# Optimization experiments

Hardware: AMD Instinct MI355X
Metric: run time of the kernel (lower is better)

Reference implementation:

```python
import jax, jax.numpy as jnp
import numpy as np

H_IMG, W_IMG = 32, 32   # image_size -> seq_len = 1024
NH, HD, D = 8, 32, 256  # num_heads, head_dim, d_model
B = 8


def _relative_positions(h, w):
    # Swin-style relative position index table, [h*w, h*w] int32
    y = np.arange(h); x = np.arange(w)
    coords = np.stack(np.meshgrid(y, x, indexing='ij')).reshape(2, -1)  # [2, S]
    rel = coords[:, :, None] - coords[:, None, :]                      # [2, S, S]
    rel = rel.transpose(1, 2, 0).astype(np.int64)                      # [S, S, 2]
    rel[:, :, 0] += h - 1
    rel[:, :, 1] += w - 1
    rel[:, :, 0] *= 2 * w - 1
    return np.int32(rel.sum(-1))                                       # [S, S]

_POS = _relative_positions(H_IMG, W_IMG)


def setup_inputs() -> dict:
    key = jax.random.key(0)
    ks = jax.random.split(key, 8)
    S = H_IMG * W_IMG
    return {
        'inputs_q': jax.random.normal(ks[0], (B, S, D), jnp.float32),
        'inputs_kv': jax.random.normal(ks[1], (B, S, D), jnp.float32),
        'Wq': jax.random.normal(ks[2], (D, NH, HD), jnp.float32) / np.sqrt(D),
        'bq': jnp.zeros((NH, HD), jnp.float32),
        'Wk': jax.random.normal(ks[3], (D, NH, HD), jnp.float32) / np.sqrt(D),
        'bk': jnp.zeros((NH, HD), jnp.float32),
        'Wv': jax.random.normal(ks[4], (D, NH, HD), jnp.float32) / np.sqrt(D),
        'bv': jnp.zeros((NH, HD), jnp.float32),
        'rel_table': 0.02 * jax.random.normal(ks[5], ((2 * H_IMG - 1) * (2 * W_IMG - 1), NH), jnp.float32),
        'Wo': jax.random.normal(ks[6], (NH, HD, D), jnp.float32) / np.sqrt(NH * HD),
        'bo': jnp.zeros((D,), jnp.float32),
    }


def reference(inputs_q, inputs_kv, Wq, bq, Wk, bk, Wv, bv, rel_table, Wo, bo):
    pos = jnp.asarray(_POS)                                  # [S, S] int32 (constant)
    q = jnp.einsum('bsd,dhk->bshk', inputs_q, Wq) + bq       # [B, S, H, HD]
    k = jnp.einsum('bsd,dhk->bshk', inputs_kv, Wk) + bk
    v = jnp.einsum('bsd,dhk->bshk', inputs_kv, Wv) + bv
    q = q / jnp.sqrt(jnp.asarray(HD, q.dtype))
    attn = jnp.einsum('bqhd,bkhd->bhqk', q, k)               # [B, H, S, S]
    rel_bias = rel_table[pos]                                # [S, S, H]
    attn = attn + jnp.transpose(rel_bias, (2, 0, 1))[None]   # broadcast over batch
    attn = jax.nn.softmax(attn, axis=-1)
    x = jnp.einsum('bhqk,bkhd->bqhd', attn, v)               # [B, S, H, HD]
    return jnp.einsum('bqhd,hdf->bqf', x, Wo) + bo           # [B, S, D]
```

## Files before the change

### kernel.cpp

```cpp
#include <hip/hip_runtime.h>
#include <hip/hip_bf16.h>

#define B_SZ   8
#define S_LEN  1024
#define D_MOD  256
#define NHEADS 8
#define HDIM   32
#define H_IMG  32
#define W_IMG  32
#define M_ROWS (B_SZ * S_LEN)

typedef _Float16 f16x8 __attribute__((ext_vector_type(8)));
typedef _Float16 f16x4 __attribute__((ext_vector_type(4)));
typedef float    f32x4 __attribute__((ext_vector_type(4)));

__device__ inline f16x8 load8_f16(const float* p) {
    f32x4 a = *(const f32x4*)p;
    f32x4 b = *(const f32x4*)(p + 4);
    f16x8 r;
    r[0] = (_Float16)a[0]; r[1] = (_Float16)a[1];
    r[2] = (_Float16)a[2]; r[3] = (_Float16)a[3];
    r[4] = (_Float16)b[0]; r[5] = (_Float16)b[1];
    r[6] = (_Float16)b[2]; r[7] = (_Float16)b[3];
    return r;
}
__device__ inline f16x8 load8_f16(const _Float16* p) { return *(const f16x8*)p; }

__global__ __launch_bounds__(256)
void wtrans_kernel(const float* __restrict__ Wq, const float* __restrict__ Wk,
                   const float* __restrict__ Wv, const float* __restrict__ Wo,
                   _Float16* __restrict__ wt) {
    const int mi = blockIdx.x >> 3;
    const int k0 = (blockIdx.x & 7) << 5;
    const float* W = (mi == 0) ? Wq : (mi == 1) ? Wk : (mi == 2) ? Wv : Wo;
    const int n = threadIdx.x;
    const float* src = W + (size_t)k0 * 256 + n;
    _Float16* dst = wt + (size_t)mi * 65536 + (size_t)n * 256 + k0;
#pragma unroll
    for (int g = 0; g < 4; ++g) {
        f16x8 o;
#pragma unroll
        for (int j = 0; j < 8; ++j) o[j] = (_Float16)src[(size_t)(g * 8 + j) * 256];
        *(f16x8*)(dst + g * 8) = o;
    }
}

template <typename InT, typename OutT>
__device__ inline void gemm_body(const InT* __restrict__ A, const _Float16* __restrict__ Wt,
                                 const float* __restrict__ bias, OutT* __restrict__ out,
                                 float scale, int m0, int n0) {
    __shared__ _Float16 As[64][136];
    __shared__ _Float16 Bt[64][136];
    const int tid  = threadIdx.x;
    const int w    = tid >> 6;
    const int lane = tid & 63;
    const int quad = lane >> 4;
    const int l16  = lane & 15;
    const int mq   = (w & 1) * 32;
    const int nq   = (w >> 1) * 32;

    f32x4 acc[2][2];
#pragma unroll
    for (int i = 0; i < 2; ++i)
#pragma unroll
        for (int j = 0; j < 2; ++j) acc[i][j] = (f32x4){0.f, 0.f, 0.f, 0.f};

#pragma unroll
    for (int ks = 0; ks < 2; ++ks) {
        if (ks) __syncthreads();
#pragma unroll
        for (int i = 0; i < 4; ++i) {
            const int idx = i * 2048 + tid * 8;
            const int r = idx >> 7, c = idx & 127;
            *(f16x8*)(&As[r][c]) = load8_f16(A + (size_t)(m0 + r) * 256 + ks * 128 + c);
            *(f16x8*)(&Bt[r][c]) = *(const f16x8*)(Wt + (size_t)(n0 + r) * 256 + ks * 128 + c);
        }
        __syncthreads();
#pragma unroll
        for (int kk = 0; kk < 4; ++kk) {
            const int k8 = kk * 32 + quad * 8;
            f16x8 a0 = *(const f16x8*)(&As[mq + l16][k8]);
            f16x8 a1 = *(const f16x8*)(&As[mq + 16 + l16][k8]);
            f16x8 b0 = *(const f16x8*)(&Bt[nq + l16][k8]);
            f16x8 b1 = *(const f16x8*)(&Bt[nq + 16 + l16][k8]);
            acc[0][0] = __builtin_amdgcn_mfma_f32_16x16x32_f16(a0, b0, acc[0][0], 0, 0, 0);
            acc[0][1] = __builtin_amdgcn_mfma_f32_16x16x32_f16(a0, b1, acc[0][1], 0, 0, 0);
            acc[1][0] = __builtin_amdgcn_mfma_f32_16x16x32_f16(a1, b0, acc[1][0], 0, 0, 0);
            acc[1][1] = __builtin_amdgcn_mfma_f32_16x16x32_f16(a1, b1, acc[1][1], 0, 0, 0);
        }
    }

#pragma unroll
    for (int nh = 0; nh < 2; ++nh) {
        const int col = n0 + nq + nh * 16 + l16;
        const float bv = bias[col];
#pragma unroll
        for (int mh = 0; mh < 2; ++mh) {
#pragma unroll
            for (int r = 0; r < 4; ++r) {
                const int row = m0 + mq + mh * 16 + quad * 4 + r;
                out[(size_t)row * 256 + col] = (OutT)((acc[mh][nh][r] + bv) * scale);
            }
        }
    }
}

__global__ __launch_bounds__(256)
void gemm_qkv_kernel(const float* __restrict__ in_q, const float* __restrict__ in_kv,
                     const _Float16* __restrict__ wt,
                     const float* __restrict__ bq, const float* __restrict__ bk,
                     const float* __restrict__ bv, _Float16* __restrict__ outbase,
                     float qscale) {
    const int z = blockIdx.z;
    const float* A    = (z == 0) ? in_q : in_kv;
    const float* bias = (z == 0) ? bq : (z == 1) ? bk : bv;
    _Float16* out = outbase + (size_t)z * M_ROWS * 256;
    const float scale = (z == 0) ? qscale : 1.0f;
    gemm_body<float, _Float16>(A, wt + (size_t)z * 65536, bias, out, scale,
                               blockIdx.x * 64, blockIdx.y * 64);
}

__global__ __launch_bounds__(256)
void gemm_out_kernel(const _Float16* __restrict__ X, const _Float16* __restrict__ wt,
                     const float* __restrict__ bo, float* __restrict__ out) {
    gemm_body<_Float16, float>(X, wt + (size_t)3 * 65536, bo, out, 1.0f,
                               blockIdx.x * 64, blockIdx.y * 64);
}

__global__ __launch_bounds__(256)
void attn_kernel(const _Float16* __restrict__ q, const _Float16* __restrict__ k,
                 const _Float16* __restrict__ v, const float* __restrict__ rel_table,
                 _Float16* __restrict__ xout) {
    __shared__ _Float16 Vt[2][32][40];
    __shared__ _Float16 Ps[4][16][40];
    __shared__ float    bias_row[4][64];

    const int tid  = threadIdx.x;
    const int w    = tid >> 6;
    const int lane = tid & 63;
    const int quad = lane >> 4;
    const int l16  = lane & 15;
    const int b    = blockIdx.z;
    const int h    = blockIdx.y;
    const int qrow_base = blockIdx.x * 64 + w * 16;
    const int yq      = qrow_base >> 5;
    const int xq_base = qrow_base & 31;

    const f16x8 q_frag =
        *(const f16x8*)(q + ((size_t)(b * S_LEN + qrow_base + l16)) * D_MOD + h * HDIM + quad * 8);

    const _Float16* kp0 = k + ((size_t)(b * S_LEN + l16)) * D_MOD + h * HDIM + quad * 8;

    const int vkey = tid >> 3;
    const int vhd  = (tid & 7) * 4;
    const _Float16* vp = v + ((size_t)(b * S_LEN + vkey)) * D_MOD + h * HDIM + vhd;

    const float* biasp = rel_table + ((size_t)(yq + 31) * 63 + lane) * NHEADS + h;

    f32x4 o_acc0 = (f32x4){0.f, 0.f, 0.f, 0.f};
    f32x4 o_acc1 = (f32x4){0.f, 0.f, 0.f, 0.f};
    float l_part[4] = {0.f, 0.f, 0.f, 0.f};

    {
        f16x4 v4 = *(const f16x4*)vp;
        Vt[0][vhd + 0][vkey] = v4[0];
        Vt[0][vhd + 1][vkey] = v4[1];
        Vt[0][vhd + 2][vkey] = v4[2];
        Vt[0][vhd + 3][vkey] = v4[3];
    }
    if (lane < 63) bias_row[w][lane] = biasp[0];
    __syncthreads();

    for (int kt = 0; kt < S_LEN / 32; ++kt) {
        const int cur = kt & 1;
        const bool more = (kt < S_LEN / 32 - 1);

        f16x4 vnext = (f16x4){0, 0, 0, 0};
        if (more) vnext = *(const f16x4*)(vp + (size_t)(kt + 1) * 32 * D_MOD);
        float bnext = 0.f;
        if (more && lane < 63) bnext = biasp[-(ptrdiff_t)(kt + 1) * 63 * NHEADS];

        const _Float16* kp = kp0 + (size_t)kt * 32 * D_MOD;
        const f16x8 kf0 = *(const f16x8*)kp;
        const f16x8 kf1 = *(const f16x8*)(kp + (size_t)16 * D_MOD);

        const f32x4 zero = (f32x4){0.f, 0.f, 0.f, 0.f};
        f32x4 s0 = __builtin_amdgcn_mfma_f32_16x16x32_f16(q_frag, kf0, zero, 0, 0, 0);
        f32x4 s1 = __builtin_amdgcn_mfma_f32_16x16x32_f16(q_frag, kf1, zero, 0, 0, 0);

#pragma unroll
        for (int r = 0; r < 4; ++r) {
            const int xq = xq_base + quad * 4 + r;
            const float p0 = __expf(s0[r] + bias_row[w][xq - l16 + 31]);
            const float p1 = __expf(s1[r] + bias_row[w][xq - l16 + 15]);
            l_part[r] += p0 + p1;
            const int ql = quad * 4 + r;
            Ps[w][ql][l16]      = (_Float16)p0;
            Ps[w][ql][l16 + 16] = (_Float16)p1;
        }

        const f16x8 pf  = *(const f16x8*)(&Ps[w][l16][quad * 8]);
        const f16x8 vf0 = *(const f16x8*)(&Vt[cur][l16][quad * 8]);
        const f16x8 vf1 = *(const f16x8*)(&Vt[cur][l16 + 16][quad * 8]);
        o_acc0 = __builtin_amdgcn_mfma_f32_16x16x32_f16(pf, vf0, o_acc0, 0, 0, 0);
        o_acc1 = __builtin_amdgcn_mfma_f32_16x16x32_f16(pf, vf1, o_acc1, 0, 0, 0);

        if (more) {
            const int nxt = cur ^ 1;
            Vt[nxt][vhd + 0][vkey] = vnext[0];
            Vt[nxt][vhd + 1][vkey] = vnext[1];
            Vt[nxt][vhd + 2][vkey] = vnext[2];
            Vt[nxt][vhd + 3][vkey] = vnext[3];
            if (lane < 63) bias_row[w][lane] = bnext;
        }
        __syncthreads();
    }

#pragma unroll
    for (int r = 0; r < 4; ++r) {
        float l = l_part[r];
        l += __shfl_xor(l, 1);
        l += __shfl_xor(l, 2);
        l += __shfl_xor(l, 4);
        l += __shfl_xor(l, 8);
        const float inv = 1.0f / l;
        const int qg = qrow_base + quad * 4 + r;
        const size_t base = ((size_t)(b * S_LEN + qg)) * D_MOD + h * HDIM;
        xout[base + l16]      = (_Float16)(o_acc0[r] * inv);
        xout[base + l16 + 16] = (_Float16)(o_acc1[r] * inv);
    }
}

extern "C" void kernel_launch(void* const* d_in, const int* in_sizes, int n_in,
                              void* d_out, int out_size, void* d_ws, size_t ws_size,
                              hipStream_t stream) {
    const float* in_q  = (const float*)d_in[0];
    const float* in_kv = (const float*)d_in[1];
    const float* Wq    = (const float*)d_in[2];
    const float* bq    = (const float*)d_in[3];
    const float* Wk    = (const float*)d_in[4];
    const float* bk    = (const float*)d_in[5];
    const float* Wv    = (const float*)d_in[6];
    const float* bv    = (const float*)d_in[7];
    const float* rel   = (const float*)d_in[8];
    const float* Wo    = (const float*)d_in[9];
    const float* bo    = (const float*)d_in[10];
    float* out = (float*)d_out;

    _Float16* qh = (_Float16*)d_ws;
    _Float16* kh = qh + (size_t)M_ROWS * D_MOD;
    _Float16* vh = kh + (size_t)M_ROWS * D_MOD;
    _Float16* xh = vh + (size_t)M_ROWS * D_MOD;
    _Float16* wt = xh + (size_t)M_ROWS * D_MOD;

    const dim3 blk(256);
    const float qscale = 0.17677669529663687f;

    wtrans_kernel<<<dim3(32), blk, 0, stream>>>(Wq, Wk, Wv, Wo, wt);
    gemm_qkv_kernel<<<dim3(M_ROWS / 64, 4, 3), blk, 0, stream>>>(
        in_q, in_kv, wt, bq, bk, bv, qh, qscale);
    attn_kernel<<<dim3(S_LEN / 64, NHEADS, B_SZ), blk, 0, stream>>>(qh, kh, vh, rel, xh);
    gemm_out_kernel<<<dim3(M_ROWS / 64, 4), blk, 0, stream>>>(xh, wt, bo, out);
}
```

Baseline: 147.9 us.

## Transpose V in QKV GEMM, restructure attention with exp2 and MFMA row sums

The QKV GEMM now double-buffers 64-wide K slices in shared memory and writes V transposed per (batch, head), so attention can load V fragments straight from global memory without an LDS transpose or block-wide barriers. Attention processes 32 query rows per wave, folds the bias into the MFMA accumulator input, uses exp2 with log2e pre-folded into the q scale and bias, and computes row sums with an extra MFMA against a ones vector. The grid is remapped so blocks of the same batch and head land on the same XCD. Risks include higher register pressure, fewer blocks in the attention launch, and per-wave Ps/bias buffers that rely on wave-level ordering without barriers.

```diff
diff --git a/kernel.cpp b/kernel.cpp
--- a/kernel.cpp
+++ b/kernel.cpp
@@ -5,26 +5,15 @@
 #define S_LEN  1024
 #define D_MOD  256
 #define NHEADS 8
-#define HDIM   32
 #define H_IMG  32
 #define W_IMG  32
 #define M_ROWS (B_SZ * S_LEN)
+#define LOG2E  1.4426950408889634f
+#define QSCALE_LOG2E 0.2550352766751165f
 
 typedef _Float16 f16x8 __attribute__((ext_vector_type(8)));
 typedef _Float16 f16x4 __attribute__((ext_vector_type(4)));
 typedef float    f32x4 __attribute__((ext_vector_type(4)));
-
-__device__ inline f16x8 load8_f16(const float* p) {
-    f32x4 a = *(const f32x4*)p;
-    f32x4 b = *(const f32x4*)(p + 4);
-    f16x8 r;
-    r[0] = (_Float16)a[0]; r[1] = (_Float16)a[1];
-    r[2] = (_Float16)a[2]; r[3] = (_Float16)a[3];
-    r[4] = (_Float16)b[0]; r[5] = (_Float16)b[1];
-    r[6] = (_Float16)b[2]; r[7] = (_Float16)b[3];
-    return r;
-}
-__device__ inline f16x8 load8_f16(const _Float16* p) { return *(const f16x8*)p; }
 
 __global__ __launch_bounds__(256)
 void wtrans_kernel(const float* __restrict__ Wq, const float* __restrict__ Wk,
@@ -45,12 +34,25 @@
     }
 }
 
-template <typename InT, typename OutT>
+__device__ inline void ldA16(const float* p, f16x8& x0, f16x8& x1) {
+    f32x4 a = *(const f32x4*)p, b = *(const f32x4*)(p + 4);
+    f32x4 c = *(const f32x4*)(p + 8), d = *(const f32x4*)(p + 12);
+#pragma unroll
+    for (int j = 0; j < 4; ++j) {
+        x0[j] = (_Float16)a[j]; x0[4 + j] = (_Float16)b[j];
+        x1[j] = (_Float16)c[j]; x1[4 + j] = (_Float16)d[j];
+    }
+}
+__device__ inline void ldA16(const _Float16* p, f16x8& x0, f16x8& x1) {
+    x0 = *(const f16x8*)p; x1 = *(const f16x8*)(p + 8);
+}
+
+template <typename InT, typename OutT, int VT_MODE>
 __device__ inline void gemm_body(const InT* __restrict__ A, const _Float16* __restrict__ Wt,
                                  const float* __restrict__ bias, OutT* __restrict__ out,
                                  float scale, int m0, int n0) {
-    __shared__ _Float16 As[64][136];
-    __shared__ _Float16 Bt[64][136];
+    __shared__ __align__(16) _Float16 As[2][64][72];
+    __shared__ __align__(16) _Float16 Bt[2][64][72];
     const int tid  = threadIdx.x;
     const int w    = tid >> 6;
     const int lane = tid & 63;
@@ -59,6 +61,20 @@
     const int mq   = (w & 1) * 32;
     const int nq   = (w >> 1) * 32;
 
+    const int srow = tid >> 2;
+    const int scol = (tid & 3) << 4;
+    const InT* Ap = A + (size_t)(m0 + srow) * 256 + scol;
+    const _Float16* Bp = Wt + (size_t)(n0 + srow) * 256 + scol;
+
+    f16x8 a0n, a1n, b0n, b1n;
+    ldA16(Ap, a0n, a1n);
+    b0n = *(const f16x8*)Bp; b1n = *(const f16x8*)(Bp + 8);
+    *(f16x8*)(&As[0][srow][scol])     = a0n;
+    *(f16x8*)(&As[0][srow][scol + 8]) = a1n;
+    *(f16x8*)(&Bt[0][srow][scol])     = b0n;
+    *(f16x8*)(&Bt[0][srow][scol + 8]) = b1n;
+    __syncthreads();
+
     f32x4 acc[2][2];
 #pragma unroll
     for (int i = 0; i < 2; ++i)
@@ -66,40 +82,63 @@
         for (int j = 0; j < 2; ++j) acc[i][j] = (f32x4){0.f, 0.f, 0.f, 0.f};
 
 #pragma unroll
-    for (int ks = 0; ks < 2; ++ks) {
-        if (ks) __syncthreads();
-#pragma unroll
-        for (int i = 0; i < 4; ++i) {
-            const int idx = i * 2048 + tid * 8;
-            const int r = idx >> 7, c = idx & 127;
-            *(f16x8*)(&As[r][c]) = load8_f16(A + (size_t)(m0 + r) * 256 + ks * 128 + c);
-            *(f16x8*)(&Bt[r][c]) = *(const f16x8*)(Wt + (size_t)(n0 + r) * 256 + ks * 128 + c);
-        }
-        __syncthreads();
-#pragma unroll
-        for (int kk = 0; kk < 4; ++kk) {
+    for (int s = 0; s < 4; ++s) {
+        const int cur = s & 1;
+        if (s < 3) {
+            ldA16(Ap + (s + 1) * 64, a0n, a1n);
+            b0n = *(const f16x8*)(Bp + (s + 1) * 64);
+            b1n = *(const f16x8*)(Bp + (s + 1) * 64 + 8);
+        }
+#pragma unroll
+        for (int kk = 0; kk < 2; ++kk) {
             const int k8 = kk * 32 + quad * 8;
-            f16x8 a0 = *(const f16x8*)(&As[mq + l16][k8]);
-            f16x8 a1 = *(const f16x8*)(&As[mq + 16 + l16][k8]);
-            f16x8 b0 = *(const f16x8*)(&Bt[nq + l16][k8]);
-            f16x8 b1 = *(const f16x8*)(&Bt[nq + 16 + l16][k8]);
-            acc[0][0] = __builtin_amdgcn_mfma_f32_16x16x32_f16(a0, b0, acc[0][0], 0, 0, 0);
-            acc[0][1] = __builtin_amdgcn_mfma_f32_16x16x32_f16(a0, b1, acc[0][1], 0, 0, 0);
-            acc[1][0] = __builtin_amdgcn_mfma_f32_16x16x32_f16(a1, b0, acc[1][0], 0, 0, 0);
-            acc[1][1] = __builtin_amdgcn_mfma_f32_16x16x32_f16(a1, b1, acc[1][1], 0, 0, 0);
-        }
-    }
-
-#pragma unroll
-    for (int nh = 0; nh < 2; ++nh) {
-        const int col = n0 + nq + nh * 16 + l16;
-        const float bv = bias[col];
-#pragma unroll
-        for (int mh = 0; mh < 2; ++mh) {
-#pragma unroll
-            for (int r = 0; r < 4; ++r) {
-                const int row = m0 + mq + mh * 16 + quad * 4 + r;
-                out[(size_t)row * 256 + col] = (OutT)((acc[mh][nh][r] + bv) * scale);
+            f16x8 fa0 = *(const f16x8*)(&As[cur][mq + l16][k8]);
+            f16x8 fa1 = *(const f16x8*)(&As[cur][mq + 16 + l16][k8]);
+            f16x8 fb0 = *(const f16x8*)(&Bt[cur][nq + l16][k8]);
+            f16x8 fb1 = *(const f16x8*)(&Bt[cur][nq + 16 + l16][k8]);
+            acc[0][0] = __builtin_amdgcn_mfma_f32_16x16x32_f16(fa0, fb0, acc[0][0], 0, 0, 0);
+            acc[0][1] = __builtin_amdgcn_mfma_f32_16x16x32_f16(fa0, fb1, acc[0][1], 0, 0, 0);
+            acc[1][0] = __builtin_amdgcn_mfma_f32_16x16x32_f16(fa1, fb0, acc[1][0], 0, 0, 0);
+            acc[1][1] = __builtin_amdgcn_mfma_f32_16x16x32_f16(fa1, fb1, acc[1][1], 0, 0, 0);
+        }
+        if (s < 3) {
+            const int nxt = cur ^ 1;
+            *(f16x8*)(&As[nxt][srow][scol])     = a0n;
+            *(f16x8*)(&As[nxt][srow][scol + 8]) = a1n;
+            *(f16x8*)(&Bt[nxt][srow][scol])     = b0n;
+            *(f16x8*)(&Bt[nxt][srow][scol + 8]) = b1n;
+            __syncthreads();
+        }
+    }
+
+    if (VT_MODE) {
+        const int b8 = (m0 >> 10) * 8;
+#pragma unroll
+        for (int nh = 0; nh < 2; ++nh) {
+            const int col = n0 + nq + nh * 16 + l16;
+            const float bv = bias[col];
+#pragma unroll
+            for (int mh = 0; mh < 2; ++mh) {
+                const int row0 = (m0 & 1023) + mq + mh * 16 + quad * 4;
+                f16x4 pk;
+#pragma unroll
+                for (int r = 0; r < 4; ++r) pk[r] = (_Float16)((acc[mh][nh][r] + bv) * scale);
+                *(f16x4*)((_Float16*)out +
+                          ((size_t)(b8 + (col >> 5)) * 32 + (col & 31)) * 1024 + row0) = pk;
+            }
+        }
+    } else {
+#pragma unroll
+        for (int nh = 0; nh < 2; ++nh) {
+            const int col = n0 + nq + nh * 16 + l16;
+            const float bv = bias[col];
+#pragma unroll
+            for (int mh = 0; mh < 2; ++mh) {
+#pragma unroll
+                for (int r = 0; r < 4; ++r) {
+                    const int row = m0 + mq + mh * 16 + quad * 4 + r;
+                    out[(size_t)row * 256 + col] = (OutT)((acc[mh][nh][r] + bv) * scale);
+                }
             }
         }
     }
@@ -109,125 +148,128 @@
 void gemm_qkv_kernel(const float* __restrict__ in_q, const float* __restrict__ in_kv,
                      const _Float16* __restrict__ wt,
                      const float* __restrict__ bq, const float* __restrict__ bk,
-                     const float* __restrict__ bv, _Float16* __restrict__ outbase,
-                     float qscale) {
+                     const float* __restrict__ bv,
+                     _Float16* __restrict__ qh, _Float16* __restrict__ kh,
+                     _Float16* __restrict__ vt) {
     const int z = blockIdx.z;
-    const float* A    = (z == 0) ? in_q : in_kv;
-    const float* bias = (z == 0) ? bq : (z == 1) ? bk : bv;
-    _Float16* out = outbase + (size_t)z * M_ROWS * 256;
-    const float scale = (z == 0) ? qscale : 1.0f;
-    gemm_body<float, _Float16>(A, wt + (size_t)z * 65536, bias, out, scale,
-                               blockIdx.x * 64, blockIdx.y * 64);
+    const int m0 = blockIdx.x * 64, n0 = blockIdx.y * 64;
+    if (z == 0)
+        gemm_body<float, _Float16, 0>(in_q, wt, bq, qh, QSCALE_LOG2E, m0, n0);
+    else if (z == 1)
+        gemm_body<float, _Float16, 0>(in_kv, wt + 65536, bk, kh, 1.0f, m0, n0);
+    else
+        gemm_body<float, _Float16, 1>(in_kv, wt + 2 * 65536, bv, vt, 1.0f, m0, n0);
 }
 
 __global__ __launch_bounds__(256)
 void gemm_out_kernel(const _Float16* __restrict__ X, const _Float16* __restrict__ wt,
                      const float* __restrict__ bo, float* __restrict__ out) {
-    gemm_body<_Float16, float>(X, wt + (size_t)3 * 65536, bo, out, 1.0f,
-                               blockIdx.x * 64, blockIdx.y * 64);
+    gemm_body<_Float16, float, 0>(X, wt + (size_t)3 * 65536, bo, out, 1.0f,
+                                  blockIdx.x * 64, blockIdx.y * 64);
 }
 
 __global__ __launch_bounds__(256)
 void attn_kernel(const _Float16* __restrict__ q, const _Float16* __restrict__ k,
-                 const _Float16* __restrict__ v, const float* __restrict__ rel_table,
+                 const _Float16* __restrict__ vt, const float* __restrict__ rel_table,
                  _Float16* __restrict__ xout) {
-    __shared__ _Float16 Vt[2][32][40];
-    __shared__ _Float16 Ps[4][16][40];
-    __shared__ float    bias_row[4][64];
+    __shared__ __align__(16) _Float16 Ps[4][2][32][40];
+    __shared__ float bias_row[4][2][64];
 
     const int tid  = threadIdx.x;
     const int w    = tid >> 6;
     const int lane = tid & 63;
     const int quad = lane >> 4;
     const int l16  = lane & 15;
-    const int b    = blockIdx.z;
-    const int h    = blockIdx.y;
-    const int qrow_base = blockIdx.x * 64 + w * 16;
-    const int yq      = qrow_base >> 5;
-    const int xq_base = qrow_base & 31;
-
-    const f16x8 q_frag =
-        *(const f16x8*)(q + ((size_t)(b * S_LEN + qrow_base + l16)) * D_MOD + h * HDIM + quad * 8);
-
-    const _Float16* kp0 = k + ((size_t)(b * S_LEN + l16)) * D_MOD + h * HDIM + quad * 8;
-
-    const int vkey = tid >> 3;
-    const int vhd  = (tid & 7) * 4;
-    const _Float16* vp = v + ((size_t)(b * S_LEN + vkey)) * D_MOD + h * HDIM + vhd;
-
-    const float* biasp = rel_table + ((size_t)(yq + 31) * 63 + lane) * NHEADS + h;
-
-    f32x4 o_acc0 = (f32x4){0.f, 0.f, 0.f, 0.f};
-    f32x4 o_acc1 = (f32x4){0.f, 0.f, 0.f, 0.f};
-    float l_part[4] = {0.f, 0.f, 0.f, 0.f};
-
-    {
-        f16x4 v4 = *(const f16x4*)vp;
-        Vt[0][vhd + 0][vkey] = v4[0];
-        Vt[0][vhd + 1][vkey] = v4[1];
-        Vt[0][vhd + 2][vkey] = v4[2];
-        Vt[0][vhd + 3][vkey] = v4[3];
-    }
-    if (lane < 63) bias_row[w][lane] = biasp[0];
-    __syncthreads();
+
+    const int n     = blockIdx.x;
+    const int xcd   = n & 7;
+    const int local = n >> 3;
+    const int bh    = xcd * 8 + (local & 7);
+    const int qc    = local >> 3;
+    const int b     = bh >> 3, h = bh & 7;
+    const int qrow_base = qc * 128 + w * 32;
+    const int yq = qrow_base >> 5;
+
+    const _Float16* qp = q + ((size_t)(b * S_LEN + qrow_base + l16)) * D_MOD + h * 32 + quad * 8;
+    const f16x8 qf0 = *(const f16x8*)(qp);
+    const f16x8 qf1 = *(const f16x8*)(qp + 16 * D_MOD);
+    const _Float16* kp = k + ((size_t)(b * S_LEN + l16)) * D_MOD + h * 32 + quad * 8;
+    const _Float16* vp = vt + ((size_t)(bh * 32 + l16)) * S_LEN + quad * 8;
+    const float* bp = rel_table + ((size_t)(yq + 31) * 63 + lane) * NHEADS + h;
+
+    f16x8 ones;
+#pragma unroll
+    for (int j = 0; j < 8; ++j) ones[j] = (_Float16)1.0f;
+
+    f32x4 o00 = {0.f,0.f,0.f,0.f}, o01 = {0.f,0.f,0.f,0.f};
+    f32x4 o10 = {0.f,0.f,0.f,0.f}, o11 = {0.f,0.f,0.f,0.f};
+    f32x4 ol0 = {0.f,0.f,0.f,0.f}, ol1 = {0.f,0.f,0.f,0.f};
+
+    if (lane < 63) bias_row[w][0][lane] = bp[0] * LOG2E;
+    f16x8 kf0 = *(const f16x8*)(kp);
+    f16x8 kf1 = *(const f16x8*)(kp + 16 * D_MOD);
+    f16x8 vf0 = *(const f16x8*)(vp);
+    f16x8 vf1 = *(const f16x8*)(vp + 16 * S_LEN);
 
     for (int kt = 0; kt < S_LEN / 32; ++kt) {
-        const int cur = kt & 1;
+        const int cur = kt & 1, nxt = cur ^ 1;
+        f16x8 nk0, nk1, nv0, nv1;
+        float nb = 0.f;
         const bool more = (kt < S_LEN / 32 - 1);
-
-        f16x4 vnext = (f16x4){0, 0, 0, 0};
-        if (more) vnext = *(const f16x4*)(vp + (size_t)(kt + 1) * 32 * D_MOD);
-        float bnext = 0.f;
-        if (more && lane < 63) bnext = biasp[-(ptrdiff_t)(kt + 1) * 63 * NHEADS];
-
-        const _Float16* kp = kp0 + (size_t)kt * 32 * D_MOD;
-        const f16x8 kf0 = *(const f16x8*)kp;
-        const f16x8 kf1 = *(const f16x8*)(kp + (size_t)16 * D_MOD);
-
-        const f32x4 zero = (f32x4){0.f, 0.f, 0.f, 0.f};
-        f32x4 s0 = __builtin_amdgcn_mfma_f32_16x16x32_f16(q_frag, kf0, zero, 0, 0, 0);
-        f32x4 s1 = __builtin_amdgcn_mfma_f32_16x16x32_f16(q_frag, kf1, zero, 0, 0, 0);
-
+        if (more) {
+            const _Float16* kq = kp + (size_t)(kt + 1) * 32 * D_MOD;
+            nk0 = *(const f16x8*)(kq);
+            nk1 = *(const f16x8*)(kq + 16 * D_MOD);
+            const _Float16* vq = vp + (kt + 1) * 32;
+            nv0 = *(const f16x8*)(vq);
+            nv1 = *(const f16x8*)(vq + 16 * S_LEN);
+            if (lane < 63) nb = bp[-(ptrdiff_t)((kt + 1) * 63 * NHEADS)];
+        }
+
+#pragma unroll
+        for (int mh = 0; mh < 2; ++mh) {
+            const f16x8 qf = mh ? qf1 : qf0;
+#pragma unroll
+            for (int kh = 0; kh < 2; ++kh) {
+                const int idx0 = mh * 16 + quad * 4 - kh * 16 - l16 + 31;
+                const float* bb = &bias_row[w][cur][idx0];
+                f32x4 c; c[0] = bb[0]; c[1] = bb[1]; c[2] = bb[2]; c[3] = bb[3];
+                f32x4 s = __builtin_amdgcn_mfma_f32_16x16x32_f16(qf, kh ? kf1 : kf0, c, 0, 0, 0);
+#pragma unroll
+                for (int r = 0; r < 4; ++r)
+                    Ps[w][cur][mh * 16 + quad * 4 + r][kh * 16 + l16] =
+                        (_Float16)__builtin_amdgcn_exp2f(s[r]);
+            }
+        }
+
+        const f16x8 pf0 = *(const f16x8*)(&Ps[w][cur][l16][quad * 8]);
+        const f16x8 pf1 = *(const f16x8*)(&Ps[w][cur][16 + l16][quad * 8]);
+        o00 = __builtin_amdgcn_mfma_f32_16x16x32_f16(pf0, vf0, o00, 0, 0, 0);
+        o01 = __builtin_amdgcn_mfma_f32_16x16x32_f16(pf0, vf1, o01, 0, 0, 0);
+        o10 = __builtin_amdgcn_mfma_f32_16x16x32_f16(pf1, vf0, o10, 0, 0, 0);
+        o11 = __builtin_amdgcn_mfma_f32_16x16x32_f16(pf1, vf1, o11, 0, 0, 0);
+        ol0 = __builtin_amdgcn_mfma_f32_16x16x32_f16(pf0, ones, ol0, 0, 0, 0);
+        ol1 = __builtin_amdgcn_mfma_f32_16x16x32_f16(pf1, ones, ol1, 0, 0, 0);
+
+        if (more) {
+            if (lane < 63) bias_row[w][nxt][lane] = nb * LOG2E;
+            kf0 = nk0; kf1 = nk1; vf0 = nv0; vf1 = nv1;
+        }
+    }
+
+#pragma unroll
+    for (int mh = 0; mh < 2; ++mh) {
+        const f32x4 oa = mh ? o10 : o00;
+        const f32x4 ob = mh ? o11 : o01;
+        const f32x4 ll = mh ? ol1 : ol0;
 #pragma unroll
         for (int r = 0; r < 4; ++r) {
-            const int xq = xq_base + quad * 4 + r;
-            const float p0 = __expf(s0[r] + bias_row[w][xq - l16 + 31]);
-            const float p1 = __expf(s1[r] + bias_row[w][xq - l16 + 15]);
-            l_part[r] += p0 + p1;
-            const int ql = quad * 4 + r;
-            Ps[w][ql][l16]      = (_Float16)p0;
-            Ps[w][ql][l16 + 16] = (_Float16)p1;
-        }
-
-        const f16x8 pf  = *(const f16x8*)(&Ps[w][l16][quad * 8]);
-        const f16x8 vf0 = *(const f16x8*)(&Vt[cur][l16][quad * 8]);
-        const f16x8 vf1 = *(const f16x8*)(&Vt[cur][l16 + 16][quad * 8]);
-        o_acc0 = __builtin_amdgcn_mfma_f32_16x16x32_f16(pf, vf0, o_acc0, 0, 0, 0);
-        o_acc1 = __builtin_amdgcn_mfma_f32_16x16x32_f16(pf, vf1, o_acc1, 0, 0, 0);
-
-        if (more) {
-            const int nxt = cur ^ 1;
-            Vt[nxt][vhd + 0][vkey] = vnext[0];
-            Vt[nxt][vhd + 1][vkey] = vnext[1];
-            Vt[nxt][vhd + 2][vkey] = vnext[2];
-            Vt[nxt][vhd + 3][vkey] = vnext[3];
-            if (lane < 63) bias_row[w][lane] = bnext;
-        }
-        __syncthreads();
-    }
-
-#pragma unroll
-    for (int r = 0; r < 4; ++r) {
-        float l = l_part[r];
-        l += __shfl_xor(l, 1);
-        l += __shfl_xor(l, 2);
-        l += __shfl_xor(l, 4);
-        l += __shfl_xor(l, 8);
-        const float inv = 1.0f / l;
-        const int qg = qrow_base + quad * 4 + r;
-        const size_t base = ((size_t)(b * S_LEN + qg)) * D_MOD + h * HDIM;
-        xout[base + l16]      = (_Float16)(o_acc0[r] * inv);
-        xout[base + l16 + 16] = (_Float16)(o_acc1[r] * inv);
+            const float inv = __builtin_amdgcn_rcpf(ll[r]);
+            const int qg = qrow_base + mh * 16 + quad * 4 + r;
+            _Float16* op = xout + ((size_t)(b * S_LEN + qg)) * D_MOD + h * 32;
+            op[l16]      = (_Float16)(oa[r] * inv);
+            op[l16 + 16] = (_Float16)(ob[r] * inv);
+        }
     }
 }
 
@@ -249,16 +291,15 @@
 
     _Float16* qh = (_Float16*)d_ws;
     _Float16* kh = qh + (size_t)M_ROWS * D_MOD;
-    _Float16* vh = kh + (size_t)M_ROWS * D_MOD;
-    _Float16* xh = vh + (size_t)M_ROWS * D_MOD;
+    _Float16* vt = kh + (size_t)M_ROWS * D_MOD;
+    _Float16* xh = vt + (size_t)M_ROWS * D_MOD;
     _Float16* wt = xh + (size_t)M_ROWS * D_MOD;
 
     const dim3 blk(256);
-    const float qscale = 0.17677669529663687f;
 
     wtrans_kernel<<<dim3(32), blk, 0, stream>>>(Wq, Wk, Wv, Wo, wt);
     gemm_qkv_kernel<<<dim3(M_ROWS / 64, 4, 3), blk, 0, stream>>>(
-        in_q, in_kv, wt, bq, bk, bv, qh, qscale);
-    attn_kernel<<<dim3(S_LEN / 64, NHEADS, B_SZ), blk, 0, stream>>>(qh, kh, vh, rel, xh);
+        in_q, in_kv, wt, bq, bk, bv, qh, kh, vt);
+    attn_kernel<<<dim3(512), blk, 0, stream>>>(qh, kh, vt, rel, xh);
     gemm_out_kernel<<<dim3(M_ROWS / 64, 4), blk, 0, stream>>>(xh, wt, bo, out);
 }
```

New measurement: 142.9 us. 1.03x faster.
